# Performance work log

Measured on AMD Instinct MI355X. Metric: run time of the kernel, lower is better.

## Reference

```python
import jax, jax.numpy as jnp
import numpy as np
from jax import lax

FEAT_STRIDE = 16
RATIOS = np.array([0.5, 1.0, 2.0], np.float32)
SCALES = np.array([8.0, 16.0, 32.0], np.float32)
PRE_NMS, POST_NMS = 6000, 300
NMS_THRESH, MIN_SIZE, SCALE = 0.7, 16.0, 1.0


def anchor_base():
    py = px = FEAT_STRIDE / 2.0
    base = np.zeros((9, 4), np.float32)
    for i, r in enumerate(RATIOS):
        for j, s in enumerate(SCALES):
            h = FEAT_STRIDE * s * np.sqrt(r)
            w = FEAT_STRIDE * s * np.sqrt(1.0 / r)
            base[i * 3 + j] = [px - w / 2.0, py - h / 2.0, px + w / 2.0, py + h / 2.0]
    return jnp.asarray(base)


def all_anchors(h, w):
    base = anchor_base()  # (9,4)
    sy = jnp.arange(h, dtype=jnp.float32) * FEAT_STRIDE
    sx = jnp.arange(w, dtype=jnp.float32) * FEAT_STRIDE
    yy, xx = jnp.meshgrid(sy, sx, indexing='ij')
    shift = jnp.stack([xx.ravel(), yy.ravel(), xx.ravel(), yy.ravel()], axis=1)  # (hw,4)
    return (shift[:, None, :] + base[None, :, :]).reshape(-1, 4)  # (hw*9,4)


def conv2d(x, w, b):
    y = lax.conv_general_dilated(x, w, (1, 1), 'SAME',
                                 dimension_numbers=('NCHW', 'OIHW', 'NCHW'))
    return y + b[None, :, None, None]


def loc2bbox(anchor, loc):
    aw = anchor[:, 2] - anchor[:, 0]
    ah = anchor[:, 3] - anchor[:, 1]
    ax = anchor[:, 0] + 0.5 * aw
    ay = anchor[:, 1] + 0.5 * ah
    cx = loc[:, 0] * aw + ax
    cy = loc[:, 1] * ah + ay
    w = jnp.exp(loc[:, 2]) * aw
    h = jnp.exp(loc[:, 3]) * ah
    return jnp.stack([cx - 0.5 * w, cy - 0.5 * h, cx + 0.5 * w, cy + 0.5 * h], axis=1)


def nms_fixed(boxes, scores):
    # top pre_nms by score, then greedy sequential NMS with fixed shapes
    s, order = lax.top_k(scores, PRE_NMS)
    b = boxes[order]
    areas = (b[:, 2] - b[:, 0]) * (b[:, 3] - b[:, 1])
    idx = jnp.arange(PRE_NMS)

    def body(i, keep):
        xx1 = jnp.maximum(b[i, 0], b[:, 0])
        yy1 = jnp.maximum(b[i, 1], b[:, 1])
        xx2 = jnp.minimum(b[i, 2], b[:, 2])
        yy2 = jnp.minimum(b[i, 3], b[:, 3])
        inter = jnp.clip(xx2 - xx1, 0.0) * jnp.clip(yy2 - yy1, 0.0)
        iou = inter / (areas[i] + areas - inter + 1e-9)
        suppress = (iou > NMS_THRESH) & (idx > i) & keep[i]
        return keep & ~suppress

    keep = lax.fori_loop(0, PRE_NMS, body, jnp.isfinite(s))
    vals, sel = lax.top_k(jnp.where(keep, s, -jnp.inf), POST_NMS)
    roi = b[sel]
    return jnp.where(jnp.isfinite(vals)[:, None], roi, 0.0)  # (POST_NMS,4)


def proposal(loc, fg, anchor, img_h, img_w):
    roi = loc2bbox(anchor, loc)
    roi = jnp.stack([jnp.clip(roi[:, 0], 0.0, img_w), jnp.clip(roi[:, 1], 0.0, img_h),
                     jnp.clip(roi[:, 2], 0.0, img_w), jnp.clip(roi[:, 3], 0.0, img_h)], axis=1)
    ms = MIN_SIZE * SCALE
    valid = ((roi[:, 2] - roi[:, 0]) >= ms) & ((roi[:, 3] - roi[:, 1]) >= ms)
    return nms_fixed(roi, jnp.where(valid, fg, -jnp.inf))


def setup_inputs() -> dict:
    key = jax.random.key(0)
    ks = jax.random.split(key, 4)
    return {
        'x': jax.random.normal(ks[0], (8, 512, 50, 76), jnp.float32),
        'conv1_w': jax.random.normal(ks[1], (512, 512, 3, 3), jnp.float32) * 0.01,
        'conv1_b': jnp.zeros((512,), jnp.float32),
        'score_w': jax.random.normal(ks[2], (18, 512, 1, 1), jnp.float32) * 0.01,
        'score_b': jnp.zeros((18,), jnp.float32),
        'loc_w': jax.random.normal(ks[3], (36, 512, 1, 1), jnp.float32) * 0.01,
        'loc_b': jnp.zeros((36,), jnp.float32),
        'img_h': 800,
        'img_w': 1216,
    }


def reference(x, conv1_w, conv1_b, score_w, score_b, loc_w, loc_b, img_h, img_w):
    b, c, h, w = x.shape
    anchor = all_anchors(h, w)  # (h*w*9,4)
    feat = jax.nn.relu(conv2d(x, conv1_w, conv1_b))
    rpn_locs = conv2d(feat, loc_w, loc_b).transpose(0, 2, 3, 1).reshape(b, -1, 4)
    rpn_scores = conv2d(feat, score_w, score_b).transpose(0, 2, 3, 1)
    sm = jax.nn.softmax(rpn_scores.reshape(b, h, w, 9, 2), axis=4)
    fg = sm[..., 1].reshape(b, -1)
    rpn_scores = rpn_scores.reshape(b, -1, 2)
    rois = jax.vmap(lambda l, f: proposal(l, f, anchor, float(img_h), float(img_w)))(rpn_locs, fg)
    rois = rois.reshape(-1, 4)  # (b*POST_NMS,4)
    return rpn_locs, rpn_scores, rois, anchor
```

## Files before the change

### kernel.cpp

```cpp
#include <hip/hip_runtime.h>
#include <stdint.h>
#include <math.h>

typedef unsigned long long u64;
typedef unsigned int u32;
typedef _Float16 half8 __attribute__((ext_vector_type(8)));
typedef float f32x4 __attribute__((ext_vector_type(4)));

#define CC   512
#define HH   50
#define WW2  76
#define PP   3800
#define NB   8
#define NA   34200
#define PRE  6000
#define POST 300
#define MWORDS 96
#define NPAD 8192
#define SCHUNK 1069


__device__ __forceinline__ u32 skey(float f) {
    u32 u = __float_as_uint(f);
    return (u & 0x80000000u) ? ~u : (u | 0x80000000u);
}

__device__ __forceinline__ float4 anchor_at(int p, int a) {
    const float rv[3] = {0.5f, 1.0f, 2.0f};
    const float sv[3] = {8.0f, 16.0f, 32.0f};
    int ri = a / 3, si = a % 3;
    float s16 = 16.0f * sv[si];
    float hh = s16 * sqrtf(rv[ri]);
    float ww = s16 * sqrtf(1.0f / rv[ri]);
    float bx1 = 8.0f - 0.5f * ww, by1 = 8.0f - 0.5f * hh;
    float bx2 = 8.0f + 0.5f * ww, by2 = 8.0f + 0.5f * hh;
    float sx = (float)((p % WW2) * 16);
    float sy = (float)((p / WW2) * 16);
    return make_float4(sx + bx1, sy + by1, sx + bx2, sy + by2);
}

__device__ __forceinline__ int lds_slot(int m, int j) {
    return (((m >> 4) * 64) + ((m & 15) ^ ((4 * (j & 1)) | (8 * (j >> 1)))) + (j << 4)) << 3;
}

__global__ void k_split_x(const float* __restrict__ x, _Float16* __restrict__ xh,
                          _Float16* __restrict__ xl) {
    __shared__ float S[32][33];
    int zim = blockIdx.z;
    int p0 = blockIdx.x * 32, c0 = blockIdx.y * 32;
    int tx = threadIdx.x, ty0 = threadIdx.y;
    const float* xi = x + (size_t)zim * CC * PP;
#pragma unroll
    for (int yy = 0; yy < 32; yy += 8) {
        int cty = c0 + ty0 + yy, ptx = p0 + tx;
        S[ty0 + yy][tx] = (ptx < PP) ? xi[(size_t)cty * PP + ptx] : 0.f;
    }
    __syncthreads();
#pragma unroll
    for (int yy = 0; yy < 32; yy += 8) {
        int p = p0 + ty0 + yy;
        if (p < PP) {
            float v = S[tx][ty0 + yy];
            _Float16 h = (_Float16)v;
            float r = v - (float)h;
            size_t o = (size_t)(zim * PP + p) * 512 + c0 + tx;
            xh[o] = h;
            xl[o] = (_Float16)(r * 2048.0f);
        }
    }
}

__global__ void k_split_w(const float* __restrict__ w, _Float16* __restrict__ wh,
                          _Float16* __restrict__ wl) {
    __shared__ float S[4608];
    int co = blockIdx.x;
    for (int t = threadIdx.x; t < 4608; t += 256) S[t] = w[(size_t)co * 4608 + t];
    __syncthreads();
    int g = co >> 4, nlo = co & 15;
    for (int e = threadIdx.x; e < 4608; e += 256) {
        int cc = e / 9, idx = e - cc * 9;
        float v = S[cc * 9 + idx];
        _Float16 h = (_Float16)v;
        float r = v - (float)h;
        int kk = (cc >> 5) * 9 + idx;
        int lane = ((cc >> 3) & 3) * 16 + nlo;
        int j = cc & 7;
        size_t d = (((size_t)g * 144 + kk) * 64 + lane) * 8 + j;
        wh[d] = h;
        wl[d] = (_Float16)(r * 2048.0f);
    }
}

__global__ void k_split_w2(const float* __restrict__ lw, const float* __restrict__ sw,
                           _Float16* __restrict__ wh2, _Float16* __restrict__ wl2) {
    int row = blockIdx.x, k = threadIdx.x;
    float v = (row < 36) ? lw[row * 512 + k] : (row < 54 ? sw[(row - 36) * 512 + k] : 0.f);
    _Float16 h = (_Float16)v;
    float r = v - (float)h;
    wh2[row * 512 + k] = h;
    wl2[row * 512 + k] = (_Float16)(r * 2048.0f);
}

__global__ __launch_bounds__(256, 2) void k_conv(
    const _Float16* __restrict__ xh, const _Float16* __restrict__ xl,
    const _Float16* __restrict__ whF, const _Float16* __restrict__ wlF,
    const float* __restrict__ bias, _Float16* __restrict__ fh,
    _Float16* __restrict__ fl, int imgbase)
{
    __shared__ _Float16 lds[2 * 8192];
    const int tid = threadIdx.x;
    const int L = blockIdx.x;
    const int X = L & 7, q = L >> 3;
    const int nt = X & 3;
    const int zim = (X >> 2) * 2 + (q >= 30 ? 1 : 0);
    const int mt = q - (q >= 30 ? 30 : 0);
    const int m0 = mt * 128, n0 = nt * 128;
    const _Float16* xhi = xh + (size_t)zim * CC * PP;
    const _Float16* xlo = xl + (size_t)zim * CC * PP;

    const int mA0 = tid >> 2, jA0 = tid & 3;
    const int mA1 = 64 + (tid >> 2);

    f32x4 acc[4][4], acc2[4][4];
#pragma unroll
    for (int i = 0; i < 4; ++i)
#pragma unroll
        for (int j = 0; j < 4; ++j) {
            acc[i][j] = f32x4{0.f, 0.f, 0.f, 0.f};
            acc2[i][j] = f32x4{0.f, 0.f, 0.f, 0.f};
        }

    uint4 pa0h, pa0l, pa1h, pa1l;

    auto ld_a = [&](int m, int idx, int c0, uint4& vh, uint4& vl) {
        int dy = idx / 3 - 1, dx = idx % 3 - 1;
        int p = m0 + m;
        int px = p % 76, py = p / 76;
        bool av = (p < PP) && ((unsigned)(py + dy) < 50u) && ((unsigned)(px + dx) < 76u);
        if (av) {
            size_t off = (size_t)(p + dy * 76 + dx) * 512 + c0 + jA0 * 8;
            vh = *(const uint4*)(xhi + off);
            vl = *(const uint4*)(xlo + off);
        } else {
            vh = make_uint4(0, 0, 0, 0);
            vl = make_uint4(0, 0, 0, 0);
        }
    };
    auto stage_load = [&](int kk) {
        int c9 = kk / 9;
        int idx = kk - c9 * 9;
        int c0 = c9 << 5;
        ld_a(mA0, idx, c0, pa0h, pa0l);
        ld_a(mA1, idx, c0, pa1h, pa1l);
    };
    const int sl0 = lds_slot(mA0, jA0);
    const int sl1 = lds_slot(mA1, jA0);
    auto stage_write = [&](int buf) {
        _Float16* Lp = lds + buf * 8192;
        *(uint4*)(Lp + sl0)        = pa0h;
        *(uint4*)(Lp + 4096 + sl0) = pa0l;
        *(uint4*)(Lp + sl1)        = pa1h;
        *(uint4*)(Lp + 4096 + sl1) = pa1l;
    };

    const int lane = tid & 63, wave = tid >> 6;
    const int wm = wave & 1, wn = wave >> 1;
    const int jr = lane >> 4;
    const int rd_off = (((lane & 15) ^ ((4 * (jr & 1)) | (8 * (jr >> 1)))) + (jr << 4)) << 3;
    const int g0 = nt * 8 + wn * 4;
    const size_t lane8 = (size_t)lane * 8;

    half8 b0h[4], b0l[4], b1h[4], b1l[4];
    auto load_b = [&](int kk, half8* bh_, half8* bl_) {
#pragma unroll
        for (int ni = 0; ni < 4; ++ni) {
            size_t off = (((size_t)(g0 + ni) * 144 + kk) * 64) * 8 + lane8;
            bh_[ni] = *(const half8*)(whF + off);
            bl_[ni] = *(const half8*)(wlF + off);
        }
    };

    auto compute = [&](int buf, const half8* bh, const half8* bl) {
        const _Float16* Lp = lds + buf * 8192;
        half8 ah[4], al[4];
#pragma unroll
        for (int mi = 0; mi < 4; ++mi) {
            int slot = (((wm * 4 + mi) * 64) << 3) + rd_off;
            ah[mi] = *(const half8*)(Lp + slot);
            al[mi] = *(const half8*)(Lp + 4096 + slot);
        }
#pragma unroll
        for (int ni = 0; ni < 4; ++ni) {
#pragma unroll
            for (int mi = 0; mi < 4; ++mi) {
                acc[mi][ni]  = __builtin_amdgcn_mfma_f32_16x16x32_f16(ah[mi], bh[ni], acc[mi][ni], 0, 0, 0);
                acc2[mi][ni] = __builtin_amdgcn_mfma_f32_16x16x32_f16(ah[mi], bl[ni], acc2[mi][ni], 0, 0, 0);
                acc2[mi][ni] = __builtin_amdgcn_mfma_f32_16x16x32_f16(al[mi], bh[ni], acc2[mi][ni], 0, 0, 0);
            }
        }
    };

    stage_load(0);
    stage_write(0);
    load_b(0, b0h, b0l);
    __syncthreads();
    for (int kk = 0; kk < 144; kk += 2) {
        stage_load(kk + 1);
        load_b(kk + 1, b1h, b1l);
        compute(0, b0h, b0l);
        stage_write(1);
        __syncthreads();
        if (kk + 2 < 144) {
            stage_load(kk + 2);
            load_b(kk + 2, b0h, b0l);
        }
        compute(1, b1h, b1l);
        if (kk + 2 < 144) stage_write(0);
        __syncthreads();
    }

    const int qq = lane >> 4, cl = lane & 15;
    const size_t rowbase = (size_t)(imgbase + zim) * PP;
#pragma unroll
    for (int ni = 0; ni < 4; ++ni) {
        int n = n0 + (wn * 4 + ni) * 16 + cl;
        float bs = bias[n];
#pragma unroll
        for (int mi = 0; mi < 4; ++mi) {
            int mb = m0 + (wm * 4 + mi) * 16 + qq * 4;
            if (mb < PP) {
#pragma unroll
                for (int r = 0; r < 4; ++r) {
                    float v = fmaxf(acc[mi][ni][r] + acc2[mi][ni][r] * (1.f / 2048.f) + bs, 0.f);
                    _Float16 h = (_Float16)v;
                    float rr = v - (float)h;
                    size_t o = (rowbase + mb + r) * 512 + n;
                    fh[o] = h;
                    fl[o] = (_Float16)(rr * 2048.0f);
                }
            }
        }
    }
}

__global__ __launch_bounds__(256) void k_hgemm_post(
    const _Float16* __restrict__ fh, const _Float16* __restrict__ fl,
    const _Float16* __restrict__ wh2, const _Float16* __restrict__ wl2,
    const float* __restrict__ lb, const float* __restrict__ sbias,
    const int* __restrict__ imh_p, const int* __restrict__ imw_p,
    float* __restrict__ out0, float* __restrict__ out1,
    float* __restrict__ boxes, float* __restrict__ scores,
    float* __restrict__ out3)
{
    const int img = blockIdx.y;
    const int p0 = blockIdx.x * 64;
    const int wave = threadIdx.x >> 6, lane = threadIdx.x & 63;
    const int q8 = (lane >> 4) * 8;
    int arow = img * PP + p0 + wave * 16 + (lane & 15);
    if (arow >= NB * PP) arow = NB * PP - 1;
    const _Float16* fhp = fh + (size_t)arow * 512 + q8;
    const _Float16* flp = fl + (size_t)arow * 512 + q8;
    const _Float16* bhp = wh2 + (size_t)(lane & 15) * 512 + q8;
    const _Float16* blp = wl2 + (size_t)(lane & 15) * 512 + q8;

    f32x4 acc[4], acc2[4];
#pragma unroll
    for (int j = 0; j < 4; ++j) {
        acc[j] = f32x4{0.f, 0.f, 0.f, 0.f};
        acc2[j] = f32x4{0.f, 0.f, 0.f, 0.f};
    }

#pragma unroll 4
    for (int k0 = 0; k0 < 512; k0 += 32) {
        half8 ah = *(const half8*)(fhp + k0);
        half8 al = *(const half8*)(flp + k0);
#pragma unroll
        for (int nf = 0; nf < 4; ++nf) {
            half8 bh = *(const half8*)(bhp + (size_t)nf * 16 * 512 + k0);
            half8 bl = *(const half8*)(blp + (size_t)nf * 16 * 512 + k0);
            acc[nf]  = __builtin_amdgcn_mfma_f32_16x16x32_f16(ah, bh, acc[nf], 0, 0, 0);
            acc2[nf] = __builtin_amdgcn_mfma_f32_16x16x32_f16(ah, bl, acc2[nf], 0, 0, 0);
            acc2[nf] = __builtin_amdgcn_mfma_f32_16x16x32_f16(al, bh, acc2[nf], 0, 0, 0);
        }
    }

    __shared__ float Ls[64][68];
    const int q = lane >> 4, cl = lane & 15;
#pragma unroll
    for (int nf = 0; nf < 4; ++nf) {
        int n = nf * 16 + cl;
        float bs = (n < 36) ? lb[n] : (n < 54 ? sbias[n - 36] : 0.f);
#pragma unroll
        for (int r = 0; r < 4; ++r) {
            int ml = wave * 16 + q * 4 + r;
            Ls[ml][n] = acc[nf][r] + acc2[nf][r] * (1.f / 2048.f) + bs;
        }
    }
    __syncthreads();

    const float fimh = (float)(*imh_p), fimw = (float)(*imw_p);
    for (int task = threadIdx.x; task < 576; task += 256) {
        int pl = task / 9, a = task - pl * 9;
        int p = p0 + pl;
        if (p >= PP) continue;
        float4 loc = *(const float4*)&Ls[pl][a * 4];
        float2 sc = make_float2(Ls[pl][36 + a * 2], Ls[pl][36 + a * 2 + 1]);
        size_t ai = (size_t)img * NA + (size_t)p * 9 + a;
        *(float4*)&out0[ai * 4] = loc;
        *(float2*)&out1[ai * 2] = sc;
        float mx = fmaxf(sc.x, sc.y);
        float e0 = expf(sc.x - mx), e1 = expf(sc.y - mx);
        float fg = e1 / (e0 + e1);
        float4 an = anchor_at(p, a);
        if (img == 0) ((float4*)out3)[p * 9 + a] = an;
        float aw = an.z - an.x, ah = an.w - an.y;
        float ax = an.x + 0.5f * aw, ay = an.y + 0.5f * ah;
        float cx = loc.x * aw + ax;
        float cy = loc.y * ah + ay;
        float wb = expf(loc.z) * aw, hb = expf(loc.w) * ah;
        float x1 = cx - 0.5f * wb, y1 = cy - 0.5f * hb;
        float x2 = cx + 0.5f * wb, y2 = cy + 0.5f * hb;
        x1 = fminf(fmaxf(x1, 0.f), fimw);
        x2 = fminf(fmaxf(x2, 0.f), fimw);
        y1 = fminf(fmaxf(y1, 0.f), fimh);
        y2 = fminf(fmaxf(y2, 0.f), fimh);
        bool valid = ((x2 - x1) >= 16.0f) && ((y2 - y1) >= 16.0f);
        ((float4*)boxes)[ai] = make_float4(x1, y1, x2, y2);
        scores[ai] = valid ? fg : -INFINITY;
    }
}


__global__ __launch_bounds__(256) void k_sel_hist(
    const float* __restrict__ scores, u32* __restrict__ ghist,
    const u32* __restrict__ gpref, int sh, int pass)
{
    __shared__ u32 wh[4][256];
    const int img = blockIdx.y, blk = blockIdx.x;
    const int tid = threadIdx.x, wv = tid >> 6;
#pragma unroll
    for (int w = 0; w < 4; ++w) wh[w][tid] = 0;
    __syncthreads();
    const u32 pmask = (pass == 0) ? 0u : (0xFFFFFFFFu << (sh + 8));
    const u32 pref = (pass == 0) ? 0u : gpref[img];
    const float4* sc4 = (const float4*)(scores + (size_t)img * NA);
    const int e40 = blk * SCHUNK;
    const int e41 = min(e40 + SCHUNK, NA / 4);
    for (int e4 = e40 + tid; e4 < e41; e4 += 256) {
        float4 s4 = sc4[e4];
        u32 kv[4] = {skey(s4.x), skey(s4.y), skey(s4.z), skey(s4.w)};
#pragma unroll
        for (int v = 0; v < 4; ++v)
            if ((kv[v] & pmask) == pref) atomicAdd(&wh[wv][(kv[v] >> sh) & 255u], 1u);
    }
    __syncthreads();
    u32 s = wh[0][tid] + wh[1][tid] + wh[2][tid] + wh[3][tid];
    if (s) atomicAdd(&ghist[img * 256 + tid], s);
}

__global__ __launch_bounds__(256) void k_sel_scan(
    u32* __restrict__ ghist, u32* __restrict__ gpref, u32* __restrict__ grem,
    int sh, int pass)
{
    __shared__ u32 A[256];
    __shared__ int s_d;
    const int img = blockIdx.x, t = threadIdx.x;
    u32 h = ghist[img * 256 + t];
    A[t] = h;
    if (t == 0) s_d = 0;
    __syncthreads();
    for (int off = 1; off < 256; off <<= 1) {
        u32 v = A[t] + ((t + off < 256) ? A[t + off] : 0u);
        __syncthreads();
        A[t] = v;
        __syncthreads();
    }
    const u32 rem = (pass == 0) ? (u32)PRE : grem[img];
    if (A[t] >= rem) atomicMax(&s_d, t);
    __syncthreads();
    if (t == 0) {
        int d = s_d;
        u32 snext = (d < 255) ? A[d + 1] : 0u;
        u32 pv = (pass == 0) ? 0u : gpref[img];
        gpref[img] = pv | ((u32)d << sh);
        grem[img] = rem - snext;
    }
    ghist[img * 256 + t] = 0;
}

__global__ __launch_bounds__(256) void k_sel_collect(
    const float* __restrict__ scores, const u32* __restrict__ gpref,
    u32* __restrict__ gccnt, u64* __restrict__ arr)
{
    __shared__ u64 lst[4288];
    __shared__ u32 s_c, s_base;
    const int img = blockIdx.y, blk = blockIdx.x;
    const int tid = threadIdx.x, lane = tid & 63;
    if (tid == 0) s_c = 0;
    __syncthreads();
    const u32 T = gpref[img];
    const float4* sc4 = (const float4*)(scores + (size_t)img * NA);
    const int e40 = blk * SCHUNK;
    const int e41 = min(e40 + SCHUNK, NA / 4);
    for (int e4 = e40 + tid; e4 < e41; e4 += 256) {
        float4 s4 = sc4[e4];
        u32 ks[4] = {skey(s4.x), skey(s4.y), skey(s4.z), skey(s4.w)};
#pragma unroll
        for (int v = 0; v < 4; ++v) {
            bool take = ks[v] >= T;
            u64 bal = __ballot(take);
            if (bal) {
                int leader = __builtin_ctzll(bal);
                u32 base = 0;
                if (lane == leader) base = atomicAdd(&s_c, (u32)__popcll(bal));
                base = (u32)__shfl((int)base, leader);
                if (take)
                    lst[base + (u32)__popcll(bal & ((1ull << lane) - 1ull))] =
                        ((u64)ks[v] << 32) | (u64)(~(u32)(e4 * 4 + v));
            }
        }
    }
    __syncthreads();
    if (tid == 0) s_base = atomicAdd(&gccnt[img], s_c);
    __syncthreads();
    const u32 base = s_base, c = s_c;
    u64* ar = arr + (size_t)img * NPAD;
    for (u32 t = tid; t < c; t += 256) {
        u32 pos = base + t;
        if (pos < NPAD) ar[pos] = lst[t];
    }
}

__global__ __launch_bounds__(1024) void k_sel_sort(
    const float* __restrict__ scores, const float4* __restrict__ boxes,
    const u64* __restrict__ arr, const u32* __restrict__ gccnt,
    float* __restrict__ sb, float4* __restrict__ bbs, float* __restrict__ areas)
{
    extern __shared__ u64 dyn[];
    u64* a = dyn;
    const int img = blockIdx.x, tid = threadIdx.x;
    u32 n = gccnt[img]; if (n > NPAD) n = NPAD;
    const u64* ar = arr + (size_t)img * NPAD;
    for (int t = tid; t < NPAD; t += 1024) a[t] = ((u32)t < n) ? ar[t] : 0ull;
    for (u32 size = 2; size <= NPAD; size <<= 1) {
        for (u32 stride = size >> 1; stride > 0; stride >>= 1) {
            __syncthreads();
            for (u32 t2 = tid; t2 < NPAD / 2; t2 += 1024) {
                u32 i = 2 * t2 - (t2 & (stride - 1));
                u32 j = i + stride;
                u64 x = a[i], y = a[j];
                bool desc = ((i & size) == 0);
                if (desc ? (x < y) : (x > y)) { a[i] = y; a[j] = x; }
            }
        }
    }
    __syncthreads();
    const float* sc = scores + (size_t)img * NA;
    for (int t2 = tid; t2 < PRE; t2 += 1024) {
        u64 v = a[t2];
        u32 e = ~(u32)v;
        float s = sc[e];
        float4 bx = boxes[(size_t)img * NA + e];
        sb[img * PRE + t2] = s;
        bbs[img * PRE + t2] = bx;
        areas[img * PRE + t2] = (bx.z - bx.x) * (bx.w - bx.y);
    }
}

__global__ __launch_bounds__(256) void k_mask(
    const float4* __restrict__ bbs, const float* __restrict__ areas,
    u64* __restrict__ mask)
{
    int img = blockIdx.z, iT = blockIdx.x, jT = blockIdx.y;
    if (jT * 256 + 255 <= iT * 64) return;
    int tid = threadIdx.x;
    __shared__ float4 jb[256];
    __shared__ float ja[256];
    int jj = jT * 256 + tid;
    jb[tid] = (jj < PRE) ? bbs[(size_t)img * PRE + jj] : make_float4(0, 0, 0, 0);
    ja[tid] = (jj < PRE) ? areas[img * PRE + jj] : 0.f;
    __syncthreads();
    int i = iT * 64 + (tid & 63);
    int jw = jT * 4 + (tid >> 6);
    if (i >= PRE) return;
    float4 bi = bbs[(size_t)img * PRE + i];
    float ai = areas[img * PRE + i];
    int j0 = (tid >> 6) * 64;
    u64 m = 0;
#pragma unroll 4
    for (int b = 0; b < 64; ++b) {
        int j = jw * 64 + b;
        if (j >= PRE) break;
        if (j > i) {
            float4 bj = jb[j0 + b];
            float xx1 = fmaxf(bi.x, bj.x), yy1 = fmaxf(bi.y, bj.y);
            float xx2 = fminf(bi.z, bj.z), yy2 = fminf(bi.w, bj.w);
            float iw = fmaxf(xx2 - xx1, 0.f), ih2 = fmaxf(yy2 - yy1, 0.f);
            float inter = iw * ih2;
            float iou = inter / (ai + ja[j0 + b] - inter + 1e-9f);
            if (iou > 0.7f) m |= (1ull << b);
        }
    }
    mask[((size_t)img * PRE + i) * MWORDS + jw] = m;
}

__global__ __launch_bounds__(128) void k_scan(
    const float* __restrict__ sb, const float4* __restrict__ bbs,
    const u64* __restrict__ mask, float* __restrict__ out2)
{
    const int img = blockIdx.x;
    const int tid = threadIdx.x;
    const int lane = tid & 63, wv = tid >> 6;
    __shared__ u64 keep[96];
    __shared__ u64 s_keptw;
    __shared__ int list[POST];
    __shared__ int s_n;
    __shared__ int s_kb[64];
    __shared__ int s_kn;

    for (int j0 = 0; j0 < PRE; j0 += 128) {
        int j = j0 + tid;
        bool alive = (j < PRE) && isfinite(sb[(size_t)img * PRE + j]);
        u64 bal = __ballot(alive);
        if (lane == 0) keep[(j0 >> 6) + wv] = bal;
    }
    if (tid == 0) { s_n = 0; keep[94] = 0; keep[95] = 0; }
    __syncthreads();

    const u64* mimg = mask + (size_t)img * PRE * MWORDS;
    for (int w = 0; w < 94; ++w) {
        if (s_n >= POST) break;
        if (wv == 0) {
            u64 myrow = mimg[(size_t)(w * 64 + lane) * MWORDS + w];
            u64 cur = keep[w];
            u64 keptw = 0;
            while (cur) {
                int b = __builtin_ctzll(cur);
                keptw |= 1ull << b;
                u64 row = __shfl(myrow, b);
                u64 hi = (b >= 63) ? 0ull : (~0ull << (b + 1));
                cur &= ~row & hi;
            }
            if (lane == 0) s_keptw = keptw;
        }
        __syncthreads();
        u64 keptw = s_keptw;
        if (tid < 64) {
            bool has = (keptw >> tid) & 1ull;
            u64 bal = __ballot(has);
            if (has) s_kb[__popcll(bal & ((1ull << tid) - 1ull))] = w * 64 + tid;
            if (tid == 0) s_kn = __popcll(keptw);
        }
        if (tid == 0) {
            int n = s_n;
            u64 bits = keptw;
            while (bits && n < POST) {
                int b = __builtin_ctzll(bits);
                bits &= bits - 1;
                list[n++] = w * 64 + b;
            }
            s_n = n;
        }
        __syncthreads();
        int kn = s_kn;
        int v = w + 1 + tid;
        if (v < 94 && kn) {
            u64 supp = 0;
            int t = 0;
            for (; t + 4 <= kn; t += 4) {
                u64 a0 = mimg[(size_t)s_kb[t] * MWORDS + v];
                u64 a1 = mimg[(size_t)s_kb[t + 1] * MWORDS + v];
                u64 a2 = mimg[(size_t)s_kb[t + 2] * MWORDS + v];
                u64 a3 = mimg[(size_t)s_kb[t + 3] * MWORDS + v];
                supp |= a0 | a1 | a2 | a3;
            }
            for (; t < kn; ++t) supp |= mimg[(size_t)s_kb[t] * MWORDS + v];
            keep[v] &= ~supp;
        }
        __syncthreads();
    }
    __syncthreads();
    int n = s_n;
    for (int e = tid; e < POST; e += 128) {
        float4 bx = (e < n) ? bbs[(size_t)img * PRE + list[e]] : make_float4(0, 0, 0, 0);
        *(float4*)&out2[((size_t)img * POST + e) * 4] = bx;
    }
}

extern "C" void kernel_launch(void* const* d_in, const int* in_sizes, int n_in,
                              void* d_out, int out_size, void* d_ws, size_t ws_size,
                              hipStream_t stream)
{
    const float* x     = (const float*)d_in[0];
    const float* w1    = (const float*)d_in[1];
    const float* b1    = (const float*)d_in[2];
    const float* sw    = (const float*)d_in[3];
    const float* sbias = (const float*)d_in[4];
    const float* lw    = (const float*)d_in[5];
    const float* lb    = (const float*)d_in[6];
    const int*   imh   = (const int*)d_in[7];
    const int*   imw   = (const int*)d_in[8];
    float* out = (float*)d_out;
    char* ws = (char*)d_ws;

    _Float16* wh2W = (_Float16*)(ws + 0);
    _Float16* wl2W = (_Float16*)(ws + 65536);
    _Float16* whW  = (_Float16*)(ws + 131072);
    _Float16* wlW  = (_Float16*)(ws + 4849664);
    _Float16* xhW  = (_Float16*)(ws + 9568256);
    _Float16* xlW  = (_Float16*)(ws + 25133056);
    float*    boxesW  = (float*)(ws + 17350656);
    float*    scoresW = (float*)(ws + 21728256);
    float*    sbW     = (float*)(ws + 22822656);
    float*    bbsW    = (float*)(ws + 23014656);
    float*    areasW  = (float*)(ws + 23782656);
    u32*      ghistW  = (u32*)(ws + 24000000);
    u32*      gccntW  = (u32*)(ws + 24008192);
    u32*      gprefW  = (u32*)(ws + 24008224);
    u32*      gremW   = (u32*)(ws + 24008256);
    u64*      arrW    = (u64*)(ws + 24016384);
    _Float16* fhW  = (_Float16*)(ws + 40697856);
    _Float16* flW  = (_Float16*)(ws + 71827456);
    u64*      maskW   = (u64*)(ws + 40697856);

    float* out0 = out;
    float* out1 = out + 1094400;
    float* out2 = out + 1641600;
    float* out3 = out + 1651200;

    hipLaunchKernelGGL(k_split_w, dim3(512), dim3(256), 0, stream, w1, whW, wlW);
    hipLaunchKernelGGL(k_split_w2, dim3(64), dim3(512), 0, stream, lw, sw, wh2W, wl2W);
    for (int b = 0; b < 2; ++b) {
        hipLaunchKernelGGL(k_split_x, dim3(119, 16, 4), dim3(32, 8), 0, stream,
                           x + (size_t)b * 4 * CC * PP, xhW, xlW);
        hipLaunchKernelGGL(k_conv, dim3(480), dim3(256), 0, stream,
                           xhW, xlW, whW, wlW, b1, fhW, flW, b * 4);
    }
    hipMemsetAsync(ws + 24000000, 0, 8224, stream);
    hipLaunchKernelGGL(k_hgemm_post, dim3(60, NB), dim3(256), 0, stream,
                       fhW, flW, wh2W, wl2W, lb, sbias, imh, imw,
                       out0, out1, boxesW, scoresW, out3);
    for (int pass = 0; pass < 4; ++pass) {
        int sh = 24 - 8 * pass;
        hipLaunchKernelGGL(k_sel_hist, dim3(8, NB), dim3(256), 0, stream,
                           scoresW, ghistW, gprefW, sh, pass);
        hipLaunchKernelGGL(k_sel_scan, dim3(NB), dim3(256), 0, stream,
                           ghistW, gprefW, gremW, sh, pass);
    }
    hipLaunchKernelGGL(k_sel_collect, dim3(8, NB), dim3(256), 0, stream,
                       scoresW, gprefW, gccntW, arrW);
    hipLaunchKernelGGL(k_sel_sort, dim3(NB), dim3(1024), NPAD * 8, stream,
                       scoresW, (const float4*)boxesW, arrW, gccntW,
                       sbW, (float4*)bbsW, areasW);
    hipLaunchKernelGGL(k_mask, dim3(94, 24, NB), dim3(256), 0, stream,
                       (const float4*)bbsW, areasW, maskW);
    hipLaunchKernelGGL(k_scan, dim3(NB), dim3(128), 0, stream,
                       sbW, (const float4*)bbsW, maskW, out2);
}
```

Measured before the change: 911.1 us.

## Restructure NMS scan to pull suppression from kept list per word

The greedy NMS scan kernel no longer pushes suppression bits forward into all later words after each 64-box word. Instead, for each word it ORs that column of the mask over the boxes already kept (at most 300), spread across 256 threads and reduced with wave shuffles. This cuts the per-word work from up to 94 columns times the kept count down to one column, and drops one barrier per iteration. The selection scratch buffers are also moved to a new workspace offset and their memset is hoisted to the start, which may let it run earlier in the stream.

```diff
diff --git a/kernel.cpp b/kernel.cpp
--- a/kernel.cpp
+++ b/kernel.cpp
@@ -504,35 +504,44 @@
     mask[((size_t)img * PRE + i) * MWORDS + jw] = m;
 }
 
-__global__ __launch_bounds__(128) void k_scan(
+__global__ __launch_bounds__(256) void k_scan(
     const float* __restrict__ sb, const float4* __restrict__ bbs,
     const u64* __restrict__ mask, float* __restrict__ out2)
 {
     const int img = blockIdx.x;
     const int tid = threadIdx.x;
     const int lane = tid & 63, wv = tid >> 6;
-    __shared__ u64 keep[96];
-    __shared__ u64 s_keptw;
+    __shared__ u64 alive[94];
     __shared__ int list[POST];
     __shared__ int s_n;
-    __shared__ int s_kb[64];
-    __shared__ int s_kn;
-
-    for (int j0 = 0; j0 < PRE; j0 += 128) {
+    __shared__ u64 wred[4];
+
+    for (int j0 = 0; j0 < 94 * 64; j0 += 256) {
         int j = j0 + tid;
-        bool alive = (j < PRE) && isfinite(sb[(size_t)img * PRE + j]);
-        u64 bal = __ballot(alive);
-        if (lane == 0) keep[(j0 >> 6) + wv] = bal;
-    }
-    if (tid == 0) { s_n = 0; keep[94] = 0; keep[95] = 0; }
+        bool al = (j < PRE) && isfinite(sb[(size_t)img * PRE + j]);
+        u64 bal = __ballot(al);
+        if (lane == 0) alive[(j0 >> 6) + wv] = bal;
+    }
+    if (tid == 0) s_n = 0;
     __syncthreads();
 
     const u64* mimg = mask + (size_t)img * PRE * MWORDS;
     for (int w = 0; w < 94; ++w) {
-        if (s_n >= POST) break;
+        int n = s_n;
+        if (n >= POST) break;
+        u64 myrow = 0;
+        if (wv == 0) myrow = mimg[(size_t)(w * 64 + lane) * MWORDS + w];
+        u64 loc = 0;
+        for (int t = tid; t < n; t += 256)
+            loc |= mimg[(size_t)list[t] * MWORDS + w];
+#pragma unroll
+        for (int off = 32; off > 0; off >>= 1)
+            loc |= __shfl_down(loc, off);
+        if (lane == 0) wred[wv] = loc;
+        __syncthreads();
         if (wv == 0) {
-            u64 myrow = mimg[(size_t)(w * 64 + lane) * MWORDS + w];
-            u64 cur = keep[w];
+            u64 supp = wred[0] | wred[1] | wred[2] | wred[3];
+            u64 cur = alive[w] & ~supp;
             u64 keptw = 0;
             while (cur) {
                 int b = __builtin_ctzll(cur);
@@ -541,47 +550,22 @@
                 u64 hi = (b >= 63) ? 0ull : (~0ull << (b + 1));
                 cur &= ~row & hi;
             }
-            if (lane == 0) s_keptw = keptw;
+            if (lane == 0) {
+                int nn = n;
+                u64 bits = keptw;
+                while (bits && nn < POST) {
+                    int bb = __builtin_ctzll(bits);
+                    bits &= bits - 1;
+                    list[nn++] = w * 64 + bb;
+                }
+                s_n = nn;
+            }
         }
         __syncthreads();
-        u64 keptw = s_keptw;
-        if (tid < 64) {
-            bool has = (keptw >> tid) & 1ull;
-            u64 bal = __ballot(has);
-            if (has) s_kb[__popcll(bal & ((1ull << tid) - 1ull))] = w * 64 + tid;
-            if (tid == 0) s_kn = __popcll(keptw);
-        }
-        if (tid == 0) {
-            int n = s_n;
-            u64 bits = keptw;
-            while (bits && n < POST) {
-                int b = __builtin_ctzll(bits);
-                bits &= bits - 1;
-                list[n++] = w * 64 + b;
-            }
-            s_n = n;
-        }
-        __syncthreads();
-        int kn = s_kn;
-        int v = w + 1 + tid;
-        if (v < 94 && kn) {
-            u64 supp = 0;
-            int t = 0;
-            for (; t + 4 <= kn; t += 4) {
-                u64 a0 = mimg[(size_t)s_kb[t] * MWORDS + v];
-                u64 a1 = mimg[(size_t)s_kb[t + 1] * MWORDS + v];
-                u64 a2 = mimg[(size_t)s_kb[t + 2] * MWORDS + v];
-                u64 a3 = mimg[(size_t)s_kb[t + 3] * MWORDS + v];
-                supp |= a0 | a1 | a2 | a3;
-            }
-            for (; t < kn; ++t) supp |= mimg[(size_t)s_kb[t] * MWORDS + v];
-            keep[v] &= ~supp;
-        }
-        __syncthreads();
     }
     __syncthreads();
     int n = s_n;
-    for (int e = tid; e < POST; e += 128) {
+    for (int e = tid; e < POST; e += 256) {
         float4 bx = (e < n) ? bbs[(size_t)img * PRE + list[e]] : make_float4(0, 0, 0, 0);
         *(float4*)&out2[((size_t)img * POST + e) * 4] = bx;
     }
@@ -614,19 +598,21 @@
     float*    sbW     = (float*)(ws + 22822656);
     float*    bbsW    = (float*)(ws + 23014656);
     float*    areasW  = (float*)(ws + 23782656);
-    u32*      ghistW  = (u32*)(ws + 24000000);
-    u32*      gccntW  = (u32*)(ws + 24008192);
-    u32*      gprefW  = (u32*)(ws + 24008224);
-    u32*      gremW   = (u32*)(ws + 24008256);
-    u64*      arrW    = (u64*)(ws + 24016384);
     _Float16* fhW  = (_Float16*)(ws + 40697856);
     _Float16* flW  = (_Float16*)(ws + 71827456);
     u64*      maskW   = (u64*)(ws + 40697856);
+    u32*      ghistW  = (u32*)(ws + 109581056);
+    u32*      gccntW  = (u32*)(ws + 109589248);
+    u32*      gprefW  = (u32*)(ws + 109589280);
+    u32*      gremW   = (u32*)(ws + 109589312);
+    u64*      arrW    = (u64*)(ws + 109597440);
 
     float* out0 = out;
     float* out1 = out + 1094400;
     float* out2 = out + 1641600;
     float* out3 = out + 1651200;
+
+    hipMemsetAsync(ws + 109581056, 0, 8224, stream);
 
     hipLaunchKernelGGL(k_split_w, dim3(512), dim3(256), 0, stream, w1, whW, wlW);
     hipLaunchKernelGGL(k_split_w2, dim3(64), dim3(512), 0, stream, lw, sw, wh2W, wl2W);
@@ -636,7 +622,6 @@
         hipLaunchKernelGGL(k_conv, dim3(480), dim3(256), 0, stream,
                            xhW, xlW, whW, wlW, b1, fhW, flW, b * 4);
     }
-    hipMemsetAsync(ws + 24000000, 0, 8224, stream);
     hipLaunchKernelGGL(k_hgemm_post, dim3(60, NB), dim3(256), 0, stream,
                        fhW, flW, wh2W, wl2W, lb, sbias, imh, imw,
                        out0, out1, boxesW, scoresW, out3);
@@ -654,6 +639,6 @@
                        sbW, (float4*)bbsW, areasW);
     hipLaunchKernelGGL(k_mask, dim3(94, 24, NB), dim3(256), 0, stream,
                        (const float4*)bbsW, areasW, maskW);
-    hipLaunchKernelGGL(k_scan, dim3(NB), dim3(128), 0, stream,
+    hipLaunchKernelGGL(k_scan, dim3(NB), dim3(256), 0, stream,
                        sbW, (const float4*)bbsW, maskW, out2);
 }
```

After: 906.7 us. About the same (-0.5%).
